# Performance work log

Hardware: AMD Instinct MI355X
Metric: run time of the kernel (lower is better)

## Reference

```python
import jax, jax.numpy as jnp
import numpy as np
from jax import lax

FACTOR = 2
BLUR_K = [1.0, 3.0, 3.0, 1.0]

def _make_kernel(k, factor):
    k = jnp.asarray(k, dtype=jnp.float32)
    k = k[None, :] * k[:, None]          # outer product -> [4,4]
    k = k / jnp.sum(k)
    return k * (factor ** 2)

def setup_inputs() -> dict:
    key = jax.random.key(0)
    x = jax.random.normal(key, (32, 512, 512, 1), dtype=jnp.float32)  # NHWC, C must be 1
    kernel = _make_kernel(BLUR_K, FACTOR)                              # [4,4]
    return {"x": x, "kernel": kernel}

def reference(x, kernel):
    # nearest-neighbor upsample by FACTOR (matches tf.image.resize nearest for integer factor)
    up = jnp.repeat(jnpp if False else jnp.repeat(x, FACTOR, axis=1), FACTOR, axis=2)
    w = kernel.reshape(1, -1, 1, 1)  # [fh=1, fw=16, in=1, out=1] (HWIO)
    out = lax.conv_general_dilated(
        up, w,
        window_strides=(1, 1),
        padding='SAME',
        dimension_numbers=('NHWC', 'HWIO', 'NHWC'),
    )
    return out
```

## Files before the change

kernel.cpp:

```cpp
#include <hip/hip_runtime.h>


#define W_IN  512
#define H_IN  512
#define NB    32
#define W_OUT 1024

__global__ __launch_bounds__(256) void upsample_blur_kernel(
    const float* __restrict__ x,
    const float* __restrict__ kern,
    float* __restrict__ out)
{
    __shared__ float row[520];

    const int rowIdx = blockIdx.x;
    const int n = rowIdx >> 9;
    const int r = rowIdx & 511;
    const int t = threadIdx.x;

    if (t < 8) {
        const int idx = (t < 4) ? t : (512 + t);
        row[idx] = 0.0f;
    }

    const float* xrow = x + (size_t)(n * H_IN + r) * W_IN;
    reinterpret_cast<float2*>(row + 4)[t] = reinterpret_cast<const float2*>(xrow)[t];

    float kf[16];
#pragma unroll
    for (int i = 0; i < 16; ++i) kf[i] = kern[i];

    float we[9], wo[8];
    we[0] = kf[0];
#pragma unroll
    for (int i = 0; i < 7; ++i) we[i + 1] = kf[2 * i + 1] + kf[2 * i + 2];
    we[8] = kf[15];
#pragma unroll
    for (int i = 0; i < 8; ++i) wo[i] = kf[2 * i] + kf[2 * i + 1];

    __syncthreads();

    float v[10];
#pragma unroll
    for (int i = 0; i < 10; ++i) v[i] = row[2 * t + i];

    float o0 = 0.f, o1 = 0.f, o2 = 0.f, o3 = 0.f;
#pragma unroll
    for (int j = 0; j < 9; ++j) o0 += we[j] * v[j];
#pragma unroll
    for (int j = 0; j < 8; ++j) o1 += wo[j] * v[j + 1];
#pragma unroll
    for (int j = 0; j < 9; ++j) o2 += we[j] * v[j + 1];
#pragma unroll
    for (int j = 0; j < 8; ++j) o3 += wo[j] * v[j + 2];

    const float4 o = make_float4(o0, o1, o2, o3);
    const size_t outRowBase = ((size_t)n * W_OUT + 2 * r) * (size_t)W_OUT;
    float4* out4a = reinterpret_cast<float4*>(out + outRowBase);
    float4* out4b = reinterpret_cast<float4*>(out + outRowBase + W_OUT);
    out4a[t] = o;
    out4b[t] = o;
}

extern "C" void kernel_launch(void* const* d_in, const int* in_sizes, int n_in,
                              void* d_out, int out_size, void* d_ws, size_t ws_size,
                              hipStream_t stream) {
    const float* x    = (const float*)d_in[0];
    const float* kern = (const float*)d_in[1];
    float* out        = (float*)d_out;

    const int numRows = NB * H_IN;
    upsample_blur_kernel<<<numRows, 256, 0, stream>>>(x, kern, out);
}
```

Before: 154.2 us.

## Process eight rows per block with vectorized loads and nontemporal stores

Each block now handles eight input rows instead of one. It loads them into shared memory with float4 loads and loops over the rows, which amortizes the kernel-weight setup and block launch overhead. Output writes use nontemporal stores to avoid polluting the cache, since the output is write-once. The block count drops 8x, which could reduce latency hiding and adds shared memory per block.

```diff
diff --git a/kernel.cpp b/kernel.cpp
--- a/kernel.cpp
+++ b/kernel.cpp
@@ -1,35 +1,45 @@
 #include <hip/hip_runtime.h>
 
 
-#define W_IN  512
-#define H_IN  512
-#define NB    32
-#define W_OUT 1024
+#define W_IN   512
+#define H_IN   512
+#define NB     32
+#define W_OUT  1024
+#define TILE_R 8
+#define ROWSTRIDE 520
+
+typedef float vf4 __attribute__((ext_vector_type(4)));
 
 __global__ __launch_bounds__(256) void upsample_blur_kernel(
     const float* __restrict__ x,
     const float* __restrict__ kern,
     float* __restrict__ out)
 {
-    __shared__ float row[520];
+    __shared__ float smem[TILE_R * ROWSTRIDE];
 
-    const int rowIdx = blockIdx.x;
-    const int n = rowIdx >> 9;
-    const int r = rowIdx & 511;
-    const int t = threadIdx.x;
+    const int t  = threadIdx.x;
+    const int g0 = blockIdx.x * TILE_R;
 
-    if (t < 8) {
-        const int idx = (t < 4) ? t : (512 + t);
-        row[idx] = 0.0f;
+    if (t < TILE_R * 8) {
+        const int rr = t >> 3;
+        const int p  = t & 7;
+        smem[rr * ROWSTRIDE + ((p < 4) ? p : 512 + p)] = 0.0f;
     }
 
-    const float* xrow = x + (size_t)(n * H_IN + r) * W_IN;
-    reinterpret_cast<float2*>(row + 4)[t] = reinterpret_cast<const float2*>(xrow)[t];
+    const vf4* __restrict__ src4 =
+        reinterpret_cast<const vf4*>(x + (size_t)g0 * W_IN);
+#pragma unroll
+    for (int i = 0; i < 4; ++i) {
+        const int idx = t + 256 * i;
+        const int rr  = idx >> 7;
+        const int c4  = idx & 127;
+        const vf4 v = src4[idx];
+        *reinterpret_cast<vf4*>(&smem[rr * ROWSTRIDE + 4 + c4 * 4]) = v;
+    }
 
     float kf[16];
 #pragma unroll
     for (int i = 0; i < 16; ++i) kf[i] = kern[i];
-
     float we[9], wo[8];
     we[0] = kf[0];
 #pragma unroll
@@ -40,26 +50,35 @@
 
     __syncthreads();
 
-    float v[10];
 #pragma unroll
-    for (int i = 0; i < 10; ++i) v[i] = row[2 * t + i];
+    for (int rr = 0; rr < TILE_R; ++rr) {
+        const float2* rowp =
+            reinterpret_cast<const float2*>(&smem[rr * ROWSTRIDE]);
+        const float2 p0 = rowp[t];
+        const float2 p1 = rowp[t + 1];
+        const float2 p2 = rowp[t + 2];
+        const float2 p3 = rowp[t + 3];
+        const float2 p4 = rowp[t + 4];
+        float v[10];
+        v[0] = p0.x; v[1] = p0.y; v[2] = p1.x; v[3] = p1.y; v[4] = p2.x;
+        v[5] = p2.y; v[6] = p3.x; v[7] = p3.y; v[8] = p4.x; v[9] = p4.y;
 
-    float o0 = 0.f, o1 = 0.f, o2 = 0.f, o3 = 0.f;
+        float o0 = 0.f, o1 = 0.f, o2 = 0.f, o3 = 0.f;
 #pragma unroll
-    for (int j = 0; j < 9; ++j) o0 += we[j] * v[j];
+        for (int j = 0; j < 9; ++j) o0 += we[j] * v[j];
 #pragma unroll
-    for (int j = 0; j < 8; ++j) o1 += wo[j] * v[j + 1];
+        for (int j = 0; j < 8; ++j) o1 += wo[j] * v[j + 1];
 #pragma unroll
-    for (int j = 0; j < 9; ++j) o2 += we[j] * v[j + 1];
+        for (int j = 0; j < 9; ++j) o2 += we[j] * v[j + 1];
 #pragma unroll
-    for (int j = 0; j < 8; ++j) o3 += wo[j] * v[j + 2];
+        for (int j = 0; j < 8; ++j) o3 += wo[j] * v[j + 2];
 
-    const float4 o = make_float4(o0, o1, o2, o3);
-    const size_t outRowBase = ((size_t)n * W_OUT + 2 * r) * (size_t)W_OUT;
-    float4* out4a = reinterpret_cast<float4*>(out + outRowBase);
-    float4* out4b = reinterpret_cast<float4*>(out + outRowBase + W_OUT);
-    out4a[t] = o;
-    out4b[t] = o;
+        vf4 o; o.x = o0; o.y = o1; o.z = o2; o.w = o3;
+        const size_t g = (size_t)(g0 + rr);
+        float* orow = out + 2 * g * (size_t)W_OUT;
+        __builtin_nontemporal_store(o, reinterpret_cast<vf4*>(orow) + t);
+        __builtin_nontemporal_store(o, reinterpret_cast<vf4*>(orow + W_OUT) + t);
+    }
 }
 
 extern "C" void kernel_launch(void* const* d_in, const int* in_sizes, int n_in,
@@ -69,6 +88,6 @@
     const float* kern = (const float*)d_in[1];
     float* out        = (float*)d_out;
 
-    const int numRows = NB * H_IN;
-    upsample_blur_kernel<<<numRows, 256, 0, stream>>>(x, kern, out);
+    const int numBlocks = NB * H_IN / TILE_R;
+    upsample_blur_kernel<<<numBlocks, 256, 0, stream>>>(x, kern, out);
 }
```

New measurement: 161.6 us. 4.8% more time.
